# Kernel optimization log

Hardware: AMD Instinct MI355X
Metric: run time of the kernel (lower is better)

## Reference

```python
import jax, jax.numpy as jnp
import numpy as np

H = 2048      # hidden_size
I = 768       # moe_intermediate_size
E = 32        # num_experts
K = 8         # num_experts_per_tok (top_k)
T = 1024      # tokens (batch * seq)


def setup_inputs() -> dict:
    key = jax.random.key(0)
    k1, k2, k3, k4 = jax.random.split(key, 4)
    return {
        "hidden_states": jax.random.normal(k1, (T, H), jnp.float32),
        "gate_weight": jax.random.normal(k2, (E, H), jnp.float32) * 0.02,
        "w13_weight": jax.random.normal(k3, (E, 2 * I, H), jnp.float32) * 0.02,
        "w2_weight": jax.random.normal(k4, (E, H, I), jnp.float32) * 0.02,
    }


def reference(hidden_states, gate_weight, w13_weight, w2_weight):
    x = hidden_states  # [T, H]
    # --- router (Qwen3MoeSparseMoeBlock gating) ---
    logits = x @ gate_weight.T                      # [T, E]
    probs = jax.nn.softmax(logits, axis=-1)
    topk_w, topk_idx = jax.lax.top_k(probs, K)      # [T, K]
    topk_w = topk_w / jnp.sum(topk_w, axis=-1, keepdims=True)  # norm_topk_prob
    # dense combine matrix [T, E]: routing weight per (token, expert), 0 if not selected
    combine = jnp.zeros((x.shape[0], E), x.dtype).at[
        jnp.arange(x.shape[0])[:, None], topk_idx
    ].add(topk_w)
    # --- expert FFNs (fused gate+up = w13, SiLU-gated, then w2 down-proj) ---
    h = jnp.einsum('th,eoh->eto', x, w13_weight)    # [E, T, 2I]
    gate, up = h[:, :, :I], h[:, :, I:]
    act = jax.nn.silu(gate) * up                    # [E, T, I]
    y = jnp.einsum('eti,ehi->eth', act, w2_weight)  # [E, T, H]
    # --- weighted combine ---
    return jnp.einsum('eth,te->th', y, combine)     # [T, H]
```

## Files before the change

### kernel.cpp

```cpp
#include <hip/hip_runtime.h>
#include <hip/hip_bf16.h>
#include <math.h>

#define T_TOK 1024
#define H_DIM 2048
#define I_DIM 768
#define E_NUM 32
#define K_TOP 8
#define BK 32
#define GRID_P 1024

typedef __bf16 bf16x8 __attribute__((ext_vector_type(8)));
typedef float  f32x4  __attribute__((ext_vector_type(4)));

__device__ __forceinline__ bf16x8 cvt2_bf16(const f32x4 a, const f32x4 b) {
    bf16x8 r;
    r[0] = (__bf16)a[0]; r[1] = (__bf16)a[1]; r[2] = (__bf16)a[2]; r[3] = (__bf16)a[3];
    r[4] = (__bf16)b[0]; r[5] = (__bf16)b[1]; r[6] = (__bf16)b[2]; r[7] = (__bf16)b[3];
    return r;
}

__device__ __forceinline__ int frag_off(int r, int kgrp8) {
    return (r >> 4) * 512 + kgrp8 * 128 + (r & 15) * 8;
}

__global__ __launch_bounds__(256) void cvtx_kernel(
    const float* __restrict__ x, __bf16* __restrict__ xb)
{
    const int i = (blockIdx.x * 256 + threadIdx.x) * 8;
    const f32x4 a = *(const f32x4*)(x + i);
    const f32x4 b = *(const f32x4*)(x + i + 4);
    *(bf16x8*)(xb + i) = cvt2_bf16(a, b);
}

__global__ __launch_bounds__(256) void router_kernel(
    const float* __restrict__ x, const float* __restrict__ gw,
    float* __restrict__ wdense, unsigned int* __restrict__ masks)
{
    const int t = blockIdx.x;
    const int tid = threadIdx.x;
    __shared__ float part[256];
    __shared__ float logits[E_NUM];
    const int e = tid & 31;
    const int chunk = tid >> 5;
    const float* xr = x + (size_t)t * H_DIM;
    const float* gr = gw + (size_t)e * H_DIM;
    const int base = chunk * (H_DIM / 8);
    float s = 0.f;
    for (int h = 0; h < H_DIM / 8; h += 4) {
        const f32x4 xv = *reinterpret_cast<const f32x4*>(xr + base + h);
        const f32x4 gv = *reinterpret_cast<const f32x4*>(gr + base + h);
        s += xv[0]*gv[0] + xv[1]*gv[1] + xv[2]*gv[2] + xv[3]*gv[3];
    }
    part[tid] = s;
    __syncthreads();
    if (tid < E_NUM) {
        float tot = 0.f;
        for (int c = 0; c < 8; ++c) tot += part[c * 32 + tid];
        logits[tid] = tot;
    }
    __syncthreads();
    if (tid == 0) {
        float l[E_NUM];
        for (int i = 0; i < E_NUM; ++i) {
            l[i] = logits[i];
            wdense[(size_t)t * E_NUM + i] = 0.f;
        }
        unsigned mask = 0;
        int   idx[K_TOP];
        float lv[K_TOP];
        for (int k = 0; k < K_TOP; ++k) {
            float best = -1e30f; int bi = 0;
            for (int i = 0; i < E_NUM; ++i)
                if (!((mask >> i) & 1u) && l[i] > best) { best = l[i]; bi = i; }
            mask |= (1u << bi); idx[k] = bi; lv[k] = best;
        }
        const float m = lv[0];
        float den = 0.f;
        for (int k = 0; k < K_TOP; ++k) den += expf(lv[k] - m);
        for (int k = 0; k < K_TOP; ++k)
            wdense[(size_t)t * E_NUM + idx[k]] = expf(lv[k] - m) / den;
        masks[t] = mask;
    }
}

__global__ __launch_bounds__(256) void count_kernel(
    const unsigned int* __restrict__ masks, int* __restrict__ cnt)
{
    const int e = blockIdx.x;
    const int tid = threadIdx.x;
    int c = 0;
    for (int t = tid; t < T_TOK; t += 256) c += (masks[t] >> e) & 1u;
    __shared__ int red[256];
    red[tid] = c; __syncthreads();
    for (int s = 128; s > 0; s >>= 1) {
        if (tid < s) red[tid] += red[tid + s];
        __syncthreads();
    }
    if (tid == 0) cnt[e] = red[0];
}

__global__ void scan_kernel(const int* __restrict__ cnt, int* __restrict__ off,
                            int* __restrict__ tbl)
{
    if (threadIdx.x == 0 && blockIdx.x == 0) {
        int r = 0, nt = 0;
        for (int e = 0; e < E_NUM; ++e) {
            off[e] = r;
            const int c = cnt[e];
            r += c;
            const int t = (c + 127) >> 7;
            for (int z = 0; z < t; ++z) tbl[1 + nt++] = (e << 8) | z;
        }
        tbl[0] = nt;
    }
}

__global__ __launch_bounds__(256) void fill_kernel(
    const unsigned int* __restrict__ masks, const float* __restrict__ wdense,
    const int* __restrict__ off, int* __restrict__ tok, float* __restrict__ wgt)
{
    const int e = blockIdx.x;
    const int tid = threadIdx.x;
    const int PER = T_TOK / 256;
    int sel[PER]; int c = 0;
    for (int i = 0; i < PER; ++i) {
        const int t = tid * PER + i;
        sel[i] = (masks[t] >> e) & 1u;
        c += sel[i];
    }
    __shared__ int s[256];
    s[tid] = c; __syncthreads();
    if (tid == 0) {
        int r = 0;
        for (int j = 0; j < 256; ++j) { int v = s[j]; s[j] = r; r += v; }
    }
    __syncthreads();
    int pos = off[e] + s[tid];
    for (int i = 0; i < PER; ++i) {
        if (sel[i]) {
            const int t = tid * PER + i;
            tok[pos] = t;
            wgt[pos] = wdense[(size_t)t * E_NUM + e];
            pos++;
        }
    }
}

#define G1_PHASE(P, Q)                                                         \
  {                                                                            \
    if (scur + 2 < NS) {                                                       \
      const int kk = (scur + 2) * BK;                                          \
      pa##P##_0 = *(const bf16x8*)(xp + kk);                                   \
      pa##P##_1 = *(const bf16x8*)(xp + kk + 8);                               \
      pb##P##_0 = *(const f32x4*)(wp + kk);                                    \
      pb##P##_1 = *(const f32x4*)(wp + kk + 4);                                \
      pb##P##_2 = *(const f32x4*)(wp + kk + 8);                                \
      pb##P##_3 = *(const f32x4*)(wp + kk + 12);                               \
    }                                                                          \
    bf16x8 af[4], bfr[4];                                                      \
    _Pragma("unroll")                                                          \
    for (int m = 0; m < 4; ++m)                                                \
      af[m] = *(const bf16x8*)&As[P][((wm >> 4) + m) * 512 + lane * 8];        \
    _Pragma("unroll")                                                          \
    for (int n = 0; n < 4; ++n)                                                \
      bfr[n] = *(const bf16x8*)&Bs[P][(wn * 4 + n) * 512 + lane * 8];          \
    _Pragma("unroll")                                                          \
    for (int m = 0; m < 4; ++m)                                                \
      _Pragma("unroll")                                                        \
      for (int n = 0; n < 4; ++n)                                              \
        acc[m][n] = __builtin_amdgcn_mfma_f32_16x16x32_bf16(af[m], bfr[n],     \
                                                            acc[m][n], 0,0,0); \
    if (scur + 1 < NS) {                                                       \
      *(bf16x8*)&As[Q][wo]       = pa##Q##_0;                                  \
      *(bf16x8*)&As[Q][wo + 128] = pa##Q##_1;                                  \
      *(bf16x8*)&Bs[Q][wo]       = cvt2_bf16(pb##Q##_0, pb##Q##_1);            \
      *(bf16x8*)&Bs[Q][wo + 128] = cvt2_bf16(pb##Q##_2, pb##Q##_3);            \
    }                                                                          \
    asm volatile("s_waitcnt lgkmcnt(0)" ::: "memory");                         \
    __builtin_amdgcn_s_barrier();                                              \
    ++scur;                                                                    \
  }

__global__ __launch_bounds__(256, 3) void gemm1_kernel(
    const __bf16* __restrict__ xb, const float* __restrict__ w13,
    const int* __restrict__ tok, const int* __restrict__ cnt,
    const int* __restrict__ off, const int* __restrict__ tbl,
    unsigned short* __restrict__ act)
{
    __shared__ __bf16 As[2][4096];
    __shared__ __bf16 Bs[2][4096];
    const int tid  = threadIdx.x;
    const int wid  = tid >> 6;
    const int lane = tid & 63;
    const int wm = (wid >> 1) * 64;
    const int wn = (wid & 1);
    const int lrow = lane & 15;
    const int sr = tid >> 1;
    const int kh = tid & 1;
    const int wo = frag_off(sr, kh * 2);
    const int NS = H_DIM / BK;

    const int W = tbl[0] * 12;
    for (int w = blockIdx.x; w < W; w += gridDim.x) {
        const int ti   = w / 12;
        const int nidx = w - ti * 12;
        const int ez = tbl[1 + ti];
        const int e  = ez >> 8;
        const int m0 = (ez & 255) * 128;
        const int c  = cnt[e];
        const int o  = off[e];
        const int n0 = nidx * 64;

        int rA = m0 + sr; rA = rA < c ? rA : c - 1;
        const __bf16* xp = xb + (size_t)tok[o + rA] * H_DIM + kh * 16;
        const int grp = sr >> 5;
        const int wrow = (grp & 1) * I_DIM + n0 + (grp >> 1) * 32 + (sr & 31);
        const float* wp = w13 + (size_t)e * (2 * I_DIM) * H_DIM
                              + (size_t)wrow * H_DIM + kh * 16;

        bf16x8 pa0_0, pa0_1, pa1_0, pa1_1;
        f32x4  pb0_0, pb0_1, pb0_2, pb0_3, pb1_0, pb1_1, pb1_2, pb1_3;
        f32x4  acc[4][4] = {};

        pa0_0 = *(const bf16x8*)(xp);
        pa0_1 = *(const bf16x8*)(xp + 8);
        pb0_0 = *(const f32x4*)(wp);
        pb0_1 = *(const f32x4*)(wp + 4);
        pb0_2 = *(const f32x4*)(wp + 8);
        pb0_3 = *(const f32x4*)(wp + 12);
        pa1_0 = *(const bf16x8*)(xp + BK);
        pa1_1 = *(const bf16x8*)(xp + BK + 8);
        pb1_0 = *(const f32x4*)(wp + BK);
        pb1_1 = *(const f32x4*)(wp + BK + 4);
        pb1_2 = *(const f32x4*)(wp + BK + 8);
        pb1_3 = *(const f32x4*)(wp + BK + 12);
        *(bf16x8*)&As[0][wo]       = pa0_0;
        *(bf16x8*)&As[0][wo + 128] = pa0_1;
        *(bf16x8*)&Bs[0][wo]       = cvt2_bf16(pb0_0, pb0_1);
        *(bf16x8*)&Bs[0][wo + 128] = cvt2_bf16(pb0_2, pb0_3);
        asm volatile("s_waitcnt lgkmcnt(0)" ::: "memory");
        __builtin_amdgcn_s_barrier();

        int scur = 0;
        for (int it = 0; it < NS; it += 2) {
            G1_PHASE(0, 1)
            G1_PHASE(1, 0)
        }

#pragma unroll
        for (int m = 0; m < 4; ++m)
#pragma unroll
            for (int n = 0; n < 2; ++n)
#pragma unroll
                for (int i = 0; i < 4; ++i) {
                    const int row = m0 + wm + m * 16 + (lane >> 4) * 4 + i;
                    if (row < c) {
                        const int icol = n0 + wn * 32 + n * 16 + lrow;
                        const float g = acc[m][n][i];
                        const float u = acc[m][n + 2][i];
                        const float a = (g / (1.f + expf(-g))) * u;
                        act[(size_t)(o + row) * I_DIM + icol] =
                            __builtin_bit_cast(unsigned short, (__bf16)a);
                    }
                }
    }
}

#define G2_PHASE(P, Q)                                                         \
  {                                                                            \
    if (scur + 2 < NS) {                                                       \
      const int kk = (scur + 2) * BK;                                          \
      qa##P##_0 = *(const bf16x8*)(ap + kk);                                   \
      qa##P##_1 = *(const bf16x8*)(ap + kk + 8);                               \
      qb##P##_0 = *(const f32x4*)(wp + kk);                                    \
      qb##P##_1 = *(const f32x4*)(wp + kk + 4);                                \
      qb##P##_2 = *(const f32x4*)(wp + kk + 8);                                \
      qb##P##_3 = *(const f32x4*)(wp + kk + 12);                               \
    }                                                                          \
    bf16x8 af[4], bfr[4];                                                      \
    _Pragma("unroll")                                                          \
    for (int m = 0; m < 4; ++m)                                                \
      af[m] = *(const bf16x8*)&As[P][((wm >> 4) + m) * 512 + lane * 8];        \
    _Pragma("unroll")                                                          \
    for (int n = 0; n < 4; ++n)                                                \
      bfr[n] = *(const bf16x8*)&Bs[P][(wn * 4 + n) * 512 + lane * 8];          \
    _Pragma("unroll")                                                          \
    for (int m = 0; m < 4; ++m)                                                \
      _Pragma("unroll")                                                        \
      for (int n = 0; n < 4; ++n)                                              \
        acc[m][n] = __builtin_amdgcn_mfma_f32_16x16x32_bf16(af[m], bfr[n],     \
                                                            acc[m][n], 0,0,0); \
    if (scur + 1 < NS) {                                                       \
      *(bf16x8*)&As[Q][wo]       = qa##Q##_0;                                  \
      *(bf16x8*)&As[Q][wo + 128] = qa##Q##_1;                                  \
      *(bf16x8*)&Bs[Q][wo]       = cvt2_bf16(qb##Q##_0, qb##Q##_1);            \
      *(bf16x8*)&Bs[Q][wo + 128] = cvt2_bf16(qb##Q##_2, qb##Q##_3);            \
    }                                                                          \
    asm volatile("s_waitcnt lgkmcnt(0)" ::: "memory");                         \
    __builtin_amdgcn_s_barrier();                                              \
    ++scur;                                                                    \
  }

__global__ __launch_bounds__(256, 3) void gemm2_kernel(
    const unsigned short* __restrict__ act, const float* __restrict__ w2,
    const int* __restrict__ tok, const float* __restrict__ wgt,
    const int* __restrict__ cnt, const int* __restrict__ off,
    const int* __restrict__ tbl, float* __restrict__ out)
{
    __shared__ __bf16 As[2][4096];
    __shared__ __bf16 Bs[2][4096];
    const int tid  = threadIdx.x;
    const int wid  = tid >> 6;
    const int lane = tid & 63;
    const int wm = (wid >> 1) * 64;
    const int wn = (wid & 1);
    const int lrow = lane & 15;
    const int sr = tid >> 1;
    const int kh = tid & 1;
    const int wo = frag_off(sr, kh * 2);
    const int NS = I_DIM / BK;

    const int W = tbl[0] * 16;
    for (int w = blockIdx.x; w < W; w += gridDim.x) {
        const int ti   = w >> 4;
        const int nidx = w & 15;
        const int ez = tbl[1 + ti];
        const int e  = ez >> 8;
        const int m0 = (ez & 255) * 128;
        const int c  = cnt[e];
        const int o  = off[e];
        const int n0 = nidx * 128;

        int rA = m0 + sr; rA = rA < c ? rA : c - 1;
        const __bf16* ap = (const __bf16*)act + (size_t)(o + rA) * I_DIM + kh * 16;
        const float* wp = w2 + (size_t)e * H_DIM * I_DIM
                             + (size_t)(n0 + sr) * I_DIM + kh * 16;

        bf16x8 qa0_0, qa0_1, qa1_0, qa1_1;
        f32x4  qb0_0, qb0_1, qb0_2, qb0_3, qb1_0, qb1_1, qb1_2, qb1_3;
        f32x4  acc[4][4] = {};

        qa0_0 = *(const bf16x8*)(ap);
        qa0_1 = *(const bf16x8*)(ap + 8);
        qb0_0 = *(const f32x4*)(wp);
        qb0_1 = *(const f32x4*)(wp + 4);
        qb0_2 = *(const f32x4*)(wp + 8);
        qb0_3 = *(const f32x4*)(wp + 12);
        qa1_0 = *(const bf16x8*)(ap + BK);
        qa1_1 = *(const bf16x8*)(ap + BK + 8);
        qb1_0 = *(const f32x4*)(wp + BK);
        qb1_1 = *(const f32x4*)(wp + BK + 4);
        qb1_2 = *(const f32x4*)(wp + BK + 8);
        qb1_3 = *(const f32x4*)(wp + BK + 12);
        *(bf16x8*)&As[0][wo]       = qa0_0;
        *(bf16x8*)&As[0][wo + 128] = qa0_1;
        *(bf16x8*)&Bs[0][wo]       = cvt2_bf16(qb0_0, qb0_1);
        *(bf16x8*)&Bs[0][wo + 128] = cvt2_bf16(qb0_2, qb0_3);
        asm volatile("s_waitcnt lgkmcnt(0)" ::: "memory");
        __builtin_amdgcn_s_barrier();

        int scur = 0;
        for (int it = 0; it < NS; it += 2) {
            G2_PHASE(0, 1)
            G2_PHASE(1, 0)
        }

#pragma unroll
        for (int m = 0; m < 4; ++m)
#pragma unroll
            for (int n = 0; n < 4; ++n)
#pragma unroll
                for (int i = 0; i < 4; ++i) {
                    const int row = m0 + wm + m * 16 + (lane >> 4) * 4 + i;
                    if (row < c) {
                        const int t = tok[o + row];
                        const float wv = wgt[o + row];
                        const int hcol = n0 + wn * 64 + n * 16 + lrow;
                        atomicAdd(&out[(size_t)t * H_DIM + hcol], wv * acc[m][n][i]);
                    }
                }
    }
}

extern "C" void kernel_launch(void* const* d_in, const int* in_sizes, int n_in,
                              void* d_out, int out_size, void* d_ws, size_t ws_size,
                              hipStream_t stream)
{
    const float* x   = (const float*)d_in[0];
    const float* gw  = (const float*)d_in[1];
    const float* w13 = (const float*)d_in[2];
    const float* w2  = (const float*)d_in[3];
    float* out = (float*)d_out;

    char* ws = (char*)d_ws;
    float*          wdense = (float*)(ws + 0x00000);
    unsigned int*   masks  = (unsigned int*)(ws + 0x20000);
    int*            cnt    = (int*)(ws + 0x21000);
    int*            off    = (int*)(ws + 0x21800);
    int*            tbl    = (int*)(ws + 0x22000);
    int*            tok    = (int*)(ws + 0x23000);
    float*          wgt    = (float*)(ws + 0x2B000);
    unsigned short* act    = (unsigned short*)(ws + 0x33000);
    __bf16*         xb     = (__bf16*)(ws + 0xC40000);

    hipMemsetAsync(d_out, 0, (size_t)out_size * sizeof(float), stream);

    cvtx_kernel<<<(T_TOK * H_DIM) / (256 * 8), 256, 0, stream>>>(x, xb);
    router_kernel<<<T_TOK, 256, 0, stream>>>(x, gw, wdense, masks);
    count_kernel<<<E_NUM, 256, 0, stream>>>(masks, cnt);
    scan_kernel<<<1, 64, 0, stream>>>(cnt, off, tbl);
    fill_kernel<<<E_NUM, 256, 0, stream>>>(masks, wdense, off, tok, wgt);
    gemm1_kernel<<<GRID_P, 256, 0, stream>>>(xb, w13, tok, cnt, off, tbl, act);
    gemm2_kernel<<<GRID_P, 256, 0, stream>>>(act, w2, tok, wgt, cnt, off, tbl, out);
}
```

Baseline: 384.3 us.

## Replace atomic scatter with per-slot buffer and combine kernel, swizzle LDS

gemm2 no longer issues float atomicAdds into the output. It writes weighted per-(token, expert) rows to a ybuf scratch, and a new combine kernel sums each token's 8 rows, which also removes the output memset. fill_kernel records each token's slot positions for that gather. LDS tile addresses are XOR-swizzled to cut bank conflicts, the launch bounds occupancy hint goes from 3 to 4, and gemm1's grid shrinks to 768 blocks. The cost is an extra 8192x2048 fp32 write and read pass through ybuf, plus one more kernel launch.

```diff
diff --git a/kernel.cpp b/kernel.cpp
--- a/kernel.cpp
+++ b/kernel.cpp
@@ -8,10 +8,11 @@
 #define E_NUM 32
 #define K_TOP 8
 #define BK 32
-#define GRID_P 1024
 
 typedef __bf16 bf16x8 __attribute__((ext_vector_type(8)));
 typedef float  f32x4  __attribute__((ext_vector_type(4)));
+
+#define MFMA16(a, b, c) __builtin_amdgcn_mfma_f32_16x16x32_bf16((a), (b), (c), 0, 0, 0)
 
 __device__ __forceinline__ bf16x8 cvt2_bf16(const f32x4 a, const f32x4 b) {
     bf16x8 r;
@@ -22,6 +23,9 @@
 
 __device__ __forceinline__ int frag_off(int r, int kgrp8) {
     return (r >> 4) * 512 + kgrp8 * 128 + (r & 15) * 8;
+}
+__device__ __forceinline__ int swz(int e) {
+    return e ^ (((e >> 8) & 3) << 3);
 }
 
 __global__ __launch_bounds__(256) void cvtx_kernel(
@@ -118,7 +122,8 @@
 
 __global__ __launch_bounds__(256) void fill_kernel(
     const unsigned int* __restrict__ masks, const float* __restrict__ wdense,
-    const int* __restrict__ off, int* __restrict__ tok, float* __restrict__ wgt)
+    const int* __restrict__ off, int* __restrict__ tok, float* __restrict__ wgt,
+    int* __restrict__ posl)
 {
     const int e = blockIdx.x;
     const int tid = threadIdx.x;
@@ -142,17 +147,19 @@
             const int t = tid * PER + i;
             tok[pos] = t;
             wgt[pos] = wdense[(size_t)t * E_NUM + e];
+            const int slot = __popc(masks[t] & ((1u << e) - 1u));
+            posl[t * K_TOP + slot] = pos;
             pos++;
         }
     }
 }
 
-#define G1_PHASE(P, Q)                                                         \
+#define GEMM_PHASE(P, Q, ATYPE)                                                \
   {                                                                            \
     if (scur + 2 < NS) {                                                       \
       const int kk = (scur + 2) * BK;                                          \
-      pa##P##_0 = *(const bf16x8*)(xp + kk);                                   \
-      pa##P##_1 = *(const bf16x8*)(xp + kk + 8);                               \
+      pa##P##_0 = *(const ATYPE*)(ap + kk);                                    \
+      pa##P##_1 = *(const ATYPE*)(ap + kk + AH);                               \
       pb##P##_0 = *(const f32x4*)(wp + kk);                                    \
       pb##P##_1 = *(const f32x4*)(wp + kk + 4);                                \
       pb##P##_2 = *(const f32x4*)(wp + kk + 8);                                \
@@ -161,28 +168,26 @@
     bf16x8 af[4], bfr[4];                                                      \
     _Pragma("unroll")                                                          \
     for (int m = 0; m < 4; ++m)                                                \
-      af[m] = *(const bf16x8*)&As[P][((wm >> 4) + m) * 512 + lane * 8];        \
+      af[m] = *(const bf16x8*)&As[P][swz(((wm >> 4) + m) * 512 + lane * 8)];   \
     _Pragma("unroll")                                                          \
     for (int n = 0; n < 4; ++n)                                                \
-      bfr[n] = *(const bf16x8*)&Bs[P][(wn * 4 + n) * 512 + lane * 8];          \
+      bfr[n] = *(const bf16x8*)&Bs[P][swz((wn * 4 + n) * 512 + lane * 8)];     \
     _Pragma("unroll")                                                          \
     for (int m = 0; m < 4; ++m)                                                \
       _Pragma("unroll")                                                        \
       for (int n = 0; n < 4; ++n)                                              \
-        acc[m][n] = __builtin_amdgcn_mfma_f32_16x16x32_bf16(af[m], bfr[n],     \
-                                                            acc[m][n], 0,0,0); \
+        acc[m][n] = MFMA16(af[m], bfr[n], acc[m][n]);                          \
     if (scur + 1 < NS) {                                                       \
-      *(bf16x8*)&As[Q][wo]       = pa##Q##_0;                                  \
-      *(bf16x8*)&As[Q][wo + 128] = pa##Q##_1;                                  \
-      *(bf16x8*)&Bs[Q][wo]       = cvt2_bf16(pb##Q##_0, pb##Q##_1);            \
-      *(bf16x8*)&Bs[Q][wo + 128] = cvt2_bf16(pb##Q##_2, pb##Q##_3);            \
+      STORE_A(Q, pa##Q##_0, pa##Q##_1)                                         \
+      *(bf16x8*)&Bs[Q][swz(wo)]       = cvt2_bf16(pb##Q##_0, pb##Q##_1);       \
+      *(bf16x8*)&Bs[Q][swz(wo + 128)] = cvt2_bf16(pb##Q##_2, pb##Q##_3);       \
     }                                                                          \
     asm volatile("s_waitcnt lgkmcnt(0)" ::: "memory");                         \
     __builtin_amdgcn_s_barrier();                                              \
     ++scur;                                                                    \
   }
 
-__global__ __launch_bounds__(256, 3) void gemm1_kernel(
+__global__ __launch_bounds__(256, 4) void gemm1_kernel(
     const __bf16* __restrict__ xb, const float* __restrict__ w13,
     const int* __restrict__ tok, const int* __restrict__ cnt,
     const int* __restrict__ off, const int* __restrict__ tbl,
@@ -200,6 +205,11 @@
     const int kh = tid & 1;
     const int wo = frag_off(sr, kh * 2);
     const int NS = H_DIM / BK;
+    const int AH = 8;
+
+#define STORE_A(Q, r0, r1)                                                     \
+      *(bf16x8*)&As[Q][swz(wo)]       = r0;                                    \
+      *(bf16x8*)&As[Q][swz(wo + 128)] = r1;
 
     const int W = tbl[0] * 12;
     for (int w = blockIdx.x; w < W; w += gridDim.x) {
@@ -213,7 +223,7 @@
         const int n0 = nidx * 64;
 
         int rA = m0 + sr; rA = rA < c ? rA : c - 1;
-        const __bf16* xp = xb + (size_t)tok[o + rA] * H_DIM + kh * 16;
+        const __bf16* ap = xb + (size_t)tok[o + rA] * H_DIM + kh * 16;
         const int grp = sr >> 5;
         const int wrow = (grp & 1) * I_DIM + n0 + (grp >> 1) * 32 + (sr & 31);
         const float* wp = w13 + (size_t)e * (2 * I_DIM) * H_DIM
@@ -223,29 +233,28 @@
         f32x4  pb0_0, pb0_1, pb0_2, pb0_3, pb1_0, pb1_1, pb1_2, pb1_3;
         f32x4  acc[4][4] = {};
 
-        pa0_0 = *(const bf16x8*)(xp);
-        pa0_1 = *(const bf16x8*)(xp + 8);
+        pa0_0 = *(const bf16x8*)(ap);
+        pa0_1 = *(const bf16x8*)(ap + 8);
         pb0_0 = *(const f32x4*)(wp);
         pb0_1 = *(const f32x4*)(wp + 4);
         pb0_2 = *(const f32x4*)(wp + 8);
         pb0_3 = *(const f32x4*)(wp + 12);
-        pa1_0 = *(const bf16x8*)(xp + BK);
-        pa1_1 = *(const bf16x8*)(xp + BK + 8);
+        pa1_0 = *(const bf16x8*)(ap + BK);
+        pa1_1 = *(const bf16x8*)(ap + BK + 8);
         pb1_0 = *(const f32x4*)(wp + BK);
         pb1_1 = *(const f32x4*)(wp + BK + 4);
         pb1_2 = *(const f32x4*)(wp + BK + 8);
         pb1_3 = *(const f32x4*)(wp + BK + 12);
-        *(bf16x8*)&As[0][wo]       = pa0_0;
-        *(bf16x8*)&As[0][wo + 128] = pa0_1;
-        *(bf16x8*)&Bs[0][wo]       = cvt2_bf16(pb0_0, pb0_1);
-        *(bf16x8*)&Bs[0][wo + 128] = cvt2_bf16(pb0_2, pb0_3);
+        STORE_A(0, pa0_0, pa0_1)
+        *(bf16x8*)&Bs[0][swz(wo)]       = cvt2_bf16(pb0_0, pb0_1);
+        *(bf16x8*)&Bs[0][swz(wo + 128)] = cvt2_bf16(pb0_2, pb0_3);
         asm volatile("s_waitcnt lgkmcnt(0)" ::: "memory");
         __builtin_amdgcn_s_barrier();
 
         int scur = 0;
         for (int it = 0; it < NS; it += 2) {
-            G1_PHASE(0, 1)
-            G1_PHASE(1, 0)
+            GEMM_PHASE(0, 1, bf16x8)
+            GEMM_PHASE(1, 0, bf16x8)
         }
 
 #pragma unroll
@@ -265,48 +274,14 @@
                     }
                 }
     }
-}
-
-#define G2_PHASE(P, Q)                                                         \
-  {                                                                            \
-    if (scur + 2 < NS) {                                                       \
-      const int kk = (scur + 2) * BK;                                          \
-      qa##P##_0 = *(const bf16x8*)(ap + kk);                                   \
-      qa##P##_1 = *(const bf16x8*)(ap + kk + 8);                               \
-      qb##P##_0 = *(const f32x4*)(wp + kk);                                    \
-      qb##P##_1 = *(const f32x4*)(wp + kk + 4);                                \
-      qb##P##_2 = *(const f32x4*)(wp + kk + 8);                                \
-      qb##P##_3 = *(const f32x4*)(wp + kk + 12);                               \
-    }                                                                          \
-    bf16x8 af[4], bfr[4];                                                      \
-    _Pragma("unroll")                                                          \
-    for (int m = 0; m < 4; ++m)                                                \
-      af[m] = *(const bf16x8*)&As[P][((wm >> 4) + m) * 512 + lane * 8];        \
-    _Pragma("unroll")                                                          \
-    for (int n = 0; n < 4; ++n)                                                \
-      bfr[n] = *(const bf16x8*)&Bs[P][(wn * 4 + n) * 512 + lane * 8];          \
-    _Pragma("unroll")                                                          \
-    for (int m = 0; m < 4; ++m)                                                \
-      _Pragma("unroll")                                                        \
-      for (int n = 0; n < 4; ++n)                                              \
-        acc[m][n] = __builtin_amdgcn_mfma_f32_16x16x32_bf16(af[m], bfr[n],     \
-                                                            acc[m][n], 0,0,0); \
-    if (scur + 1 < NS) {                                                       \
-      *(bf16x8*)&As[Q][wo]       = qa##Q##_0;                                  \
-      *(bf16x8*)&As[Q][wo + 128] = qa##Q##_1;                                  \
-      *(bf16x8*)&Bs[Q][wo]       = cvt2_bf16(qb##Q##_0, qb##Q##_1);            \
-      *(bf16x8*)&Bs[Q][wo + 128] = cvt2_bf16(qb##Q##_2, qb##Q##_3);            \
-    }                                                                          \
-    asm volatile("s_waitcnt lgkmcnt(0)" ::: "memory");                         \
-    __builtin_amdgcn_s_barrier();                                              \
-    ++scur;                                                                    \
-  }
-
-__global__ __launch_bounds__(256, 3) void gemm2_kernel(
+#undef STORE_A
+}
+
+__global__ __launch_bounds__(256, 4) void gemm2_kernel(
     const unsigned short* __restrict__ act, const float* __restrict__ w2,
     const int* __restrict__ tok, const float* __restrict__ wgt,
     const int* __restrict__ cnt, const int* __restrict__ off,
-    const int* __restrict__ tbl, float* __restrict__ out)
+    const int* __restrict__ tbl, float* __restrict__ ybuf)
 {
     __shared__ __bf16 As[2][4096];
     __shared__ __bf16 Bs[2][4096];
@@ -320,6 +295,11 @@
     const int kh = tid & 1;
     const int wo = frag_off(sr, kh * 2);
     const int NS = I_DIM / BK;
+    const int AH = 8;
+
+#define STORE_A(Q, r0, r1)                                                     \
+      *(bf16x8*)&As[Q][swz(wo)]       = r0;                                    \
+      *(bf16x8*)&As[Q][swz(wo + 128)] = r1;
 
     const int W = tbl[0] * 16;
     for (int w = blockIdx.x; w < W; w += gridDim.x) {
@@ -337,49 +317,69 @@
         const float* wp = w2 + (size_t)e * H_DIM * I_DIM
                              + (size_t)(n0 + sr) * I_DIM + kh * 16;
 
-        bf16x8 qa0_0, qa0_1, qa1_0, qa1_1;
-        f32x4  qb0_0, qb0_1, qb0_2, qb0_3, qb1_0, qb1_1, qb1_2, qb1_3;
+        bf16x8 pa0_0, pa0_1, pa1_0, pa1_1;
+        f32x4  pb0_0, pb0_1, pb0_2, pb0_3, pb1_0, pb1_1, pb1_2, pb1_3;
         f32x4  acc[4][4] = {};
 
-        qa0_0 = *(const bf16x8*)(ap);
-        qa0_1 = *(const bf16x8*)(ap + 8);
-        qb0_0 = *(const f32x4*)(wp);
-        qb0_1 = *(const f32x4*)(wp + 4);
-        qb0_2 = *(const f32x4*)(wp + 8);
-        qb0_3 = *(const f32x4*)(wp + 12);
-        qa1_0 = *(const bf16x8*)(ap + BK);
-        qa1_1 = *(const bf16x8*)(ap + BK + 8);
-        qb1_0 = *(const f32x4*)(wp + BK);
-        qb1_1 = *(const f32x4*)(wp + BK + 4);
-        qb1_2 = *(const f32x4*)(wp + BK + 8);
-        qb1_3 = *(const f32x4*)(wp + BK + 12);
-        *(bf16x8*)&As[0][wo]       = qa0_0;
-        *(bf16x8*)&As[0][wo + 128] = qa0_1;
-        *(bf16x8*)&Bs[0][wo]       = cvt2_bf16(qb0_0, qb0_1);
-        *(bf16x8*)&Bs[0][wo + 128] = cvt2_bf16(qb0_2, qb0_3);
+        pa0_0 = *(const bf16x8*)(ap);
+        pa0_1 = *(const bf16x8*)(ap + 8);
+        pb0_0 = *(const f32x4*)(wp);
+        pb0_1 = *(const f32x4*)(wp + 4);
+        pb0_2 = *(const f32x4*)(wp + 8);
+        pb0_3 = *(const f32x4*)(wp + 12);
+        pa1_0 = *(const bf16x8*)(ap + BK);
+        pa1_1 = *(const bf16x8*)(ap + BK + 8);
+        pb1_0 = *(const f32x4*)(wp + BK);
+        pb1_1 = *(const f32x4*)(wp + BK + 4);
+        pb1_2 = *(const f32x4*)(wp + BK + 8);
+        pb1_3 = *(const f32x4*)(wp + BK + 12);
+        STORE_A(0, pa0_0, pa0_1)
+        *(bf16x8*)&Bs[0][swz(wo)]       = cvt2_bf16(pb0_0, pb0_1);
+        *(bf16x8*)&Bs[0][swz(wo + 128)] = cvt2_bf16(pb0_2, pb0_3);
         asm volatile("s_waitcnt lgkmcnt(0)" ::: "memory");
         __builtin_amdgcn_s_barrier();
 
         int scur = 0;
         for (int it = 0; it < NS; it += 2) {
-            G2_PHASE(0, 1)
-            G2_PHASE(1, 0)
+            GEMM_PHASE(0, 1, bf16x8)
+            GEMM_PHASE(1, 0, bf16x8)
         }
 
 #pragma unroll
         for (int m = 0; m < 4; ++m)
 #pragma unroll
-            for (int n = 0; n < 4; ++n)
-#pragma unroll
-                for (int i = 0; i < 4; ++i) {
-                    const int row = m0 + wm + m * 16 + (lane >> 4) * 4 + i;
-                    if (row < c) {
-                        const int t = tok[o + row];
-                        const float wv = wgt[o + row];
-                        const int hcol = n0 + wn * 64 + n * 16 + lrow;
-                        atomicAdd(&out[(size_t)t * H_DIM + hcol], wv * acc[m][n][i]);
-                    }
+            for (int i = 0; i < 4; ++i) {
+                const int row = m0 + wm + m * 16 + (lane >> 4) * 4 + i;
+                if (row < c) {
+                    const float wv = wgt[o + row];
+                    float* yr = ybuf + (size_t)(o + row) * H_DIM + n0 + wn * 64 + lrow;
+#pragma unroll
+                    for (int n = 0; n < 4; ++n)
+                        yr[n * 16] = wv * acc[m][n][i];
                 }
+            }
+    }
+#undef STORE_A
+}
+
+__global__ __launch_bounds__(256) void combine_kernel(
+    const float* __restrict__ ybuf, const int* __restrict__ posl,
+    float* __restrict__ out)
+{
+    const int t = blockIdx.x;
+    int p[K_TOP];
+#pragma unroll
+    for (int s = 0; s < K_TOP; ++s) p[s] = posl[t * K_TOP + s];
+    const int h0 = threadIdx.x * 4;
+#pragma unroll
+    for (int hh = h0; hh < H_DIM; hh += 1024) {
+        f32x4 a = {0.f, 0.f, 0.f, 0.f};
+#pragma unroll
+        for (int s = 0; s < K_TOP; ++s) {
+            const f32x4 v = *(const f32x4*)(ybuf + (size_t)p[s] * H_DIM + hh);
+            a[0] += v[0]; a[1] += v[1]; a[2] += v[2]; a[3] += v[3];
+        }
+        *(f32x4*)(out + (size_t)t * H_DIM + hh) = a;
     }
 }
 
@@ -403,14 +403,15 @@
     float*          wgt    = (float*)(ws + 0x2B000);
     unsigned short* act    = (unsigned short*)(ws + 0x33000);
     __bf16*         xb     = (__bf16*)(ws + 0xC40000);
-
-    hipMemsetAsync(d_out, 0, (size_t)out_size * sizeof(float), stream);
+    int*            posl   = (int*)(ws + 0x1040000);
+    float*          ybuf   = (float*)(ws + 0x1100000);
 
     cvtx_kernel<<<(T_TOK * H_DIM) / (256 * 8), 256, 0, stream>>>(x, xb);
     router_kernel<<<T_TOK, 256, 0, stream>>>(x, gw, wdense, masks);
     count_kernel<<<E_NUM, 256, 0, stream>>>(masks, cnt);
     scan_kernel<<<1, 64, 0, stream>>>(cnt, off, tbl);
-    fill_kernel<<<E_NUM, 256, 0, stream>>>(masks, wdense, off, tok, wgt);
-    gemm1_kernel<<<GRID_P, 256, 0, stream>>>(xb, w13, tok, cnt, off, tbl, act);
-    gemm2_kernel<<<GRID_P, 256, 0, stream>>>(act, w2, tok, wgt, cnt, off, tbl, out);
-}
+    fill_kernel<<<E_NUM, 256, 0, stream>>>(masks, wdense, off, tok, wgt, posl);
+    gemm1_kernel<<<768, 256, 0, stream>>>(xb, w13, tok, cnt, off, tbl, act);
+    gemm2_kernel<<<1024, 256, 0, stream>>>(act, w2, tok, wgt, cnt, off, tbl, ybuf);
+    combine_kernel<<<T_TOK, 256, 0, stream>>>(ybuf, posl, out);
+}
```

Measured after the change: 750.3 us. +95.2%, slower.
